# Performance work log

Measured on AMD Instinct MI355X. Metric: run time of the kernel, lower is better.

Reference implementation:

```python
import jax, jax.numpy as jnp
import numpy as np

D_MODEL = 1024
NUM_HEADS = 16
D_FF = 4096
NEG_INF = -1e9


def _linear_params(key, d_in, d_out):
    kw, kb = jax.random.split(key)
    bound = 1.0 / np.sqrt(d_in)
    W = jax.random.uniform(kw, (d_in, d_out), jnp.float32, -bound, bound)
    b = jax.random.uniform(kb, (d_out,), jnp.float32, -bound, bound)
    return W, b


def setup_inputs() -> dict:
    key = jax.random.key(0)
    ks = jax.random.split(key, 8)
    B, S = 2, 2048
    x = jax.random.normal(ks[0], (B, S, D_MODEL), jnp.float32)
    # causal mask: 1 = attend, 0 = masked
    mask = jnp.tril(jnp.ones((S, S), jnp.bool_))[None, :, :]
    Wq, bq = _linear_params(ks[1], D_MODEL, D_MODEL)
    Wk, bk = _linear_params(ks[2], D_MODEL, D_MODEL)
    Wv, bv = _linear_params(ks[3], D_MODEL, D_MODEL)
    Wo, bo = _linear_params(ks[4], D_MODEL, D_MODEL)
    W1, b1 = _linear_params(ks[5], D_MODEL, D_FF)
    W2, b2 = _linear_params(ks[6], D_FF, D_MODEL)
    ln1_g = jnp.ones((D_MODEL,), jnp.float32)
    ln1_b = jnp.zeros((D_MODEL,), jnp.float32)
    ln2_g = jnp.ones((D_MODEL,), jnp.float32)
    ln2_b = jnp.zeros((D_MODEL,), jnp.float32)
    return {"x": x, "mask": mask,
            "Wq": Wq, "bq": bq, "Wk": Wk, "bk": bk, "Wv": Wv, "bv": bv,
            "Wo": Wo, "bo": bo, "W1": W1, "b1": b1, "W2": W2, "b2": b2,
            "ln1_g": ln1_g, "ln1_b": ln1_b, "ln2_g": ln2_g, "ln2_b": ln2_b}


def layer_norm(x, g, b, eps=1e-5):
    mu = jnp.mean(x, axis=-1, keepdims=True)
    var = jnp.mean(jnp.square(x - mu), axis=-1, keepdims=True)
    return (x - mu) * jax.lax.rsqrt(var + eps) * g + b


def attention(xn, mask, Wq, bq, Wk, bk, Wv, bv, Wo, bo):
    B, S, D = xn.shape
    H, dk = NUM_HEADS, D // NUM_HEADS
    q = (xn @ Wq + bq).reshape(B, S, H, dk).transpose(0, 2, 1, 3)  # [B,H,S,dk]
    k = (xn @ Wk + bk).reshape(B, S, H, dk).transpose(0, 2, 1, 3)
    v = (xn @ Wv + bv).reshape(B, S, H, dk).transpose(0, 2, 1, 3)
    scores = jnp.einsum("bhsd,bhtd->bhst", q, k) / jnp.sqrt(jnp.float32(dk))
    scores = jnp.where(mask[:, None, :, :], scores, NEG_INF)
    attn = jax.nn.softmax(scores, axis=-1)
    out = jnp.einsum("bhst,bhtd->bhsd", attn, v)  # [B,H,S,dk]
    out = out.transpose(0, 2, 1, 3).reshape(B, S, D)
    return out @ Wo + bo


def reference(x, mask, Wq, bq, Wk, bk, Wv, bv, Wo, bo, W1, b1, W2, b2,
              ln1_g, ln1_b, ln2_g, ln2_b):
    # pre-norm MHA + residual (dropout = identity at eval)
    h = x + attention(layer_norm(x, ln1_g, ln1_b), mask,
                      Wq, bq, Wk, bk, Wv, bv, Wo, bo)
    # pre-norm FFN + residual
    ff = jax.nn.relu(layer_norm(h, ln2_g, ln2_b) @ W1 + b1) @ W2 + b2
    return h + ff
```

## Files before the change

### kernel.cpp

```cpp
#include <hip/hip_runtime.h>

typedef unsigned short u16;
typedef __attribute__((ext_vector_type(8))) short    s16x8;
typedef __attribute__((ext_vector_type(8))) unsigned short u16x8;
typedef __attribute__((ext_vector_type(4))) float    f32x4;

typedef __attribute__((address_space(1))) const void gvoid_c;
typedef __attribute__((address_space(3))) void       lvoid;

__device__ __forceinline__ float b2f(u16 x) {
    return __builtin_bit_cast(float, (unsigned)x << 16);
}
__device__ __forceinline__ u16 f2bf(float f) {
    unsigned u = __builtin_bit_cast(unsigned, f);
    return (u16)((u + 0x7FFFu + ((u >> 16) & 1u)) >> 16);
}
__device__ __forceinline__ u16 f2bf_trunc(float f) {
    return (u16)(__builtin_bit_cast(unsigned, f) >> 16);
}
__device__ __forceinline__ void gld16(const void* g, void* l) {
    __builtin_amdgcn_global_load_lds((gvoid_c*)g, (lvoid*)l, 16, 0, 0);
}

__global__ __launch_bounds__(256) void transpose_all(
    const float* __restrict__ Wq, const float* __restrict__ Wk,
    const float* __restrict__ Wv, const float* __restrict__ Wo,
    const float* __restrict__ W1, const float* __restrict__ W2,
    const float* __restrict__ bq, const float* __restrict__ bk,
    const float* __restrict__ bv,
    u16* __restrict__ Wqkv_t, u16* __restrict__ Wo_t,
    u16* __restrict__ W1_t, u16* __restrict__ W2_t, float* __restrict__ bqkv)
{
    __shared__ u16 tile[32][33];
    int id = blockIdx.x;
    if (id >= 12288) {
        int i = (id - 12288) * 256 + threadIdx.x;
        bqkv[i] = (i < 1024) ? bq[i] : (i < 2048 ? bk[i - 1024] : bv[i - 2048]);
        return;
    }
    const float* src; u16* dst; int R, C, bx, by;
    if (id < 4096) {
        int m = id >> 10, r = id & 1023;
        bx = r & 31; by = r >> 5; R = 1024; C = 1024;
        src = (m == 0) ? Wq : (m == 1) ? Wk : (m == 2) ? Wv : Wo;
        dst = (m == 0) ? Wqkv_t : (m == 1) ? Wqkv_t + 1024 * 1024
            : (m == 2) ? Wqkv_t + 2048 * 1024 : Wo_t;
    } else if (id < 8192) {
        int r = id - 4096; bx = r & 127; by = r >> 7; R = 1024; C = 4096;
        src = W1; dst = W1_t;
    } else {
        int r = id - 8192; bx = r & 31; by = r >> 5; R = 4096; C = 1024;
        src = W2; dst = W2_t;
    }
    int tx = threadIdx.x & 31, ty = threadIdx.x >> 5;
    int c0 = bx * 32, r0 = by * 32;
#pragma unroll
    for (int i = 0; i < 32; i += 8)
        tile[ty + i][tx] = f2bf(src[(size_t)(r0 + ty + i) * C + c0 + tx]);
    __syncthreads();
#pragma unroll
    for (int i = 0; i < 32; i += 8)
        dst[(size_t)(c0 + ty + i) * R + r0 + tx] = tile[tx][ty + i];
}

__global__ __launch_bounds__(256) void ln_k(
    const float* __restrict__ in, const float* __restrict__ gg,
    const float* __restrict__ bb, u16* __restrict__ out)
{
    const int D = 1024;
    int row  = blockIdx.x * 4 + (threadIdx.x >> 6);
    int lane = threadIdx.x & 63;
    const float* ip = in + (size_t)row * D;
    float v[16];
#pragma unroll
    for (int cc = 0; cc < 4; cc++) {
        f32x4 t = *(const f32x4*)(ip + cc * 256 + lane * 4);
#pragma unroll
        for (int i = 0; i < 4; i++) v[cc * 4 + i] = t[i];
    }
    float s1 = 0.f, s2 = 0.f;
#pragma unroll
    for (int i = 0; i < 16; i++) { s1 += v[i]; s2 += v[i] * v[i]; }
#pragma unroll
    for (int m = 1; m < 64; m <<= 1) { s1 += __shfl_xor(s1, m); s2 += __shfl_xor(s2, m); }
    float mu   = s1 * (1.f / 1024.f);
    float var  = s2 * (1.f / 1024.f) - mu * mu;
    float rstd = rsqrtf(var + 1e-5f);
#pragma unroll
    for (int cc = 0; cc < 4; cc++) {
        int e = cc * 256 + lane * 4;
        f32x4 gv = *(const f32x4*)(gg + e);
        f32x4 bv = *(const f32x4*)(bb + e);
        u16 o[4];
#pragma unroll
        for (int i = 0; i < 4; i++)
            o[i] = f2bf((v[cc * 4 + i] - mu) * rstd * gv[i] + bv[i]);
        *(__attribute__((ext_vector_type(4))) unsigned short*)(out + (size_t)row * D + e) =
            (__attribute__((ext_vector_type(4))) unsigned short){o[0], o[1], o[2], o[3]};
    }
}

template <int BN, int RES, bool RELU, bool OUTF32>
__global__ __launch_bounds__(256) void gemm2(
    const u16* __restrict__ A, const u16* __restrict__ Bt,
    const float* __restrict__ bias, const float* __restrict__ res,
    void* __restrict__ out, int M, int N, int K)
{
    constexpr int NFR = BN / 32;
    __shared__ u16 As[2][4096];
    __shared__ u16 Bs[2][BN * 32];
    int tid = threadIdx.x, wave = tid >> 6, lane = tid & 63;
    int g = lane >> 4, c = lane & 15;
    int wm = wave >> 1, wn = wave & 1;

    int gx = gridDim.x, nwg = gx * gridDim.y;
    int id = blockIdx.y * gx + blockIdx.x;
    int swz = (id & 7) * (nwg >> 3) + (id >> 3);
    int m0 = (swz / gx) * 128, n0 = (swz % gx) * BN;

    f32x4 acc[4][NFR];
#pragma unroll
    for (int m = 0; m < 4; m++)
#pragma unroll
        for (int n = 0; n < NFR; n++) acc[m][n] = (f32x4){0, 0, 0, 0};

    int ch0 = wave * 128 + lane, ch1 = ch0 + 64;
    const u16* Ag0 = A + (size_t)(m0 + (ch0 >> 2)) * K + (ch0 & 3) * 8;
    const u16* Ag1 = A + (size_t)(m0 + (ch1 >> 2)) * K + (ch1 & 3) * 8;
    const u16* Bg0;
    const u16* Bg1 = nullptr;
    if constexpr (BN == 128) {
        Bg0 = Bt + (size_t)(n0 + (ch0 >> 2)) * K + (ch0 & 3) * 8;
        Bg1 = Bt + (size_t)(n0 + (ch1 >> 2)) * K + (ch1 & 3) * 8;
    } else {
        int chb = wave * 64 + lane;
        Bg0 = Bt + (size_t)(n0 + (chb >> 2)) * K + (chb & 3) * 8;
    }

    auto stage = [&](int buf, int kk) {
        gld16(Ag0 + kk, &As[buf][wave * 1024]);
        gld16(Ag1 + kk, &As[buf][wave * 1024 + 512]);
        if constexpr (BN == 128) {
            gld16(Bg0 + kk, &Bs[buf][wave * 1024]);
            gld16(Bg1 + kk, &Bs[buf][wave * 1024 + 512]);
        } else {
            gld16(Bg0 + kk, &Bs[buf][wave * 512]);
        }
    };

    int nt = K / 32;
    stage(0, 0);
    __syncthreads();
    int cur = 0;
    for (int t = 0; t < nt; t++) {
        if (t + 1 < nt) stage(cur ^ 1, (t + 1) * 32);
        s16x8 af[4], bfr[NFR];
#pragma unroll
        for (int m = 0; m < 4; m++)
            af[m] = *(const s16x8*)&As[cur][(wm * 64 + m * 16 + c) * 32 + g * 8];
#pragma unroll
        for (int n = 0; n < NFR; n++)
            bfr[n] = *(const s16x8*)&Bs[cur][(wn * (BN / 2) + n * 16 + c) * 32 + g * 8];
        __builtin_amdgcn_s_setprio(1);
#pragma unroll
        for (int m = 0; m < 4; m++)
#pragma unroll
            for (int n = 0; n < NFR; n++)
                acc[m][n] = __builtin_amdgcn_mfma_f32_16x16x32_bf16(af[m], bfr[n], acc[m][n], 0, 0, 0);
        __builtin_amdgcn_s_setprio(0);
        __syncthreads();
        cur ^= 1;
    }

#pragma unroll
    for (int n = 0; n < NFR; n++) {
        int col = n0 + wn * (BN / 2) + n * 16 + c;
        float bb = bias[col];
#pragma unroll
        for (int m = 0; m < 4; m++) {
#pragma unroll
            for (int j = 0; j < 4; j++) {
                int row = m0 + wm * 64 + m * 16 + g * 4 + j;
                float v = acc[m][n][j] + bb;
                if constexpr (RES == 2) v += res[(size_t)row * N + col];
                if constexpr (RELU) v = fmaxf(v, 0.f);
                if constexpr (OUTF32) ((float*)out)[(size_t)row * N + col] = v;
                else                  ((u16*)out)[(size_t)row * N + col] = f2bf(v);
            }
        }
    }
}

__global__ __launch_bounds__(256) void gemm_n64_k64(
    const u16* __restrict__ A, const u16* __restrict__ Bt,
    const float* __restrict__ bias, const float* __restrict__ res,
    float* __restrict__ out, int M, int N, int K)
{
    __shared__ u16 As[2][8192];
    __shared__ u16 Bs[2][4096];
    int tid = threadIdx.x, wave = tid >> 6, lane = tid & 63;
    int g = lane >> 4, c = lane & 15;
    int wm = wave >> 1, wn = wave & 1;

    int gx = gridDim.x, nwg = gx * gridDim.y;
    int id = blockIdx.y * gx + blockIdx.x;
    int swz = (id & 7) * (nwg >> 3) + (id >> 3);
    int m0 = (swz / gx) * 128, n0 = (swz % gx) * 64;

    f32x4 acc[4][2];
#pragma unroll
    for (int m = 0; m < 4; m++)
#pragma unroll
        for (int n = 0; n < 2; n++) acc[m][n] = (f32x4){0, 0, 0, 0};

    const u16* asrc[4];
#pragma unroll
    for (int k = 0; k < 4; k++) {
        int ch = k * 256 + tid, row = ch >> 3, c8 = ch & 7;
        asrc[k] = A + (size_t)(m0 + row) * K + ((c8 ^ (row & 7)) * 8);
    }
    const u16* bsrc[2];
#pragma unroll
    for (int k = 0; k < 2; k++) {
        int ch = k * 256 + tid, row = ch >> 3, c8 = ch & 7;
        bsrc[k] = Bt + (size_t)(n0 + row) * K + ((c8 ^ (row & 7)) * 8);
    }

    auto stage = [&](int buf, int k0) {
#pragma unroll
        for (int k = 0; k < 4; k++)
            gld16(asrc[k] + k0, &As[buf][(k * 256 + wave * 64) * 8]);
#pragma unroll
        for (int k = 0; k < 2; k++)
            gld16(bsrc[k] + k0, &Bs[buf][(k * 256 + wave * 64) * 8]);
    };

    int nt = K / 64;
    stage(0, 0);
    __syncthreads();
    int cur = 0;
    int x7 = c & 7;
    for (int t = 0; t < nt; t++) {
        if (t + 1 < nt) stage(cur ^ 1, (t + 1) * 64);
        s16x8 af[2][4], bfr[2][2];
#pragma unroll
        for (int kk = 0; kk < 2; kk++) {
#pragma unroll
            for (int m = 0; m < 4; m++)
                af[kk][m] = *(const s16x8*)&As[cur][(wm * 64 + m * 16 + c) * 64 + ((kk * 4 + g) ^ x7) * 8];
#pragma unroll
            for (int n = 0; n < 2; n++)
                bfr[kk][n] = *(const s16x8*)&Bs[cur][(wn * 32 + n * 16 + c) * 64 + ((kk * 4 + g) ^ x7) * 8];
        }
        __builtin_amdgcn_s_setprio(1);
#pragma unroll
        for (int kk = 0; kk < 2; kk++)
#pragma unroll
            for (int m = 0; m < 4; m++)
#pragma unroll
                for (int n = 0; n < 2; n++)
                    acc[m][n] = __builtin_amdgcn_mfma_f32_16x16x32_bf16(af[kk][m], bfr[kk][n], acc[m][n], 0, 0, 0);
        __builtin_amdgcn_s_setprio(0);
        __syncthreads();
        cur ^= 1;
    }

#pragma unroll
    for (int n = 0; n < 2; n++) {
        int col = n0 + wn * 32 + n * 16 + c;
        float bb = bias[col];
#pragma unroll
        for (int m = 0; m < 4; m++) {
#pragma unroll
            for (int j = 0; j < 4; j++) {
                int row = m0 + wm * 64 + m * 16 + g * 4 + j;
                out[(size_t)row * N + col] = acc[m][n][j] + bb + res[(size_t)row * N + col];
            }
        }
    }
}

__global__ __launch_bounds__(256) void v_transpose(
    const u16* __restrict__ qkv, u16* __restrict__ vt)
{
    const int S = 2048, NC = 3072;
    __shared__ u16 tile[64][72];
    int st = blockIdx.x, bh = blockIdx.y, b = bh >> 4, h = bh & 15;
    int tid = threadIdx.x;
    int i = tid >> 3, cb8 = (tid & 7) * 8;
    const u16* src = qkv + (size_t)(b * S + st * 64) * NC + 2048 + h * 64;
    u16x8 a0 = *(const u16x8*)(src + (size_t)i * NC + cb8);
    u16x8 a1 = *(const u16x8*)(src + (size_t)(i + 32) * NC + cb8);
    *(u16x8*)&tile[i][cb8]      = a0;
    *(u16x8*)&tile[i + 32][cb8] = a1;
    __syncthreads();
    int d = tid >> 3, e8 = (tid & 7) * 8;
    int m = (d & 7) * 8;
#pragma unroll
    for (int rr = 0; rr < 2; rr++) {
        int r = d + rr * 32;
        u16x8 o;
#pragma unroll
        for (int j = 0; j < 8; j++) o[j] = tile[(e8 ^ m) + j][r];
        *(u16x8*)(vt + ((size_t)bh * 64 + r) * 2048 + st * 64 + e8) = o;
    }
}

__global__ __launch_bounds__(256) void attn_fwd4(
    const u16* __restrict__ qkv, const u16* __restrict__ vt,
    u16* __restrict__ o)
{
    const int S = 2048, NC = 3072;
    __shared__ u16 Ks[2][4096];
    __shared__ u16 Vs[2][4096];
    __shared__ u16 Plds[4][16][72];
    int qp = blockIdx.x, bh = blockIdx.y, b = bh >> 4, h = bh & 15;
    int tid = threadIdx.x, wave = tid >> 6, lane = tid & 63;
    int g = lane >> 4, c = lane & 15;
    int sr = tid >> 3, scb8 = (tid & 7) * 8;
    int mS = (sr & 7) * 8;
    int mR = (c & 7) * 8;

    const u16* kbase = qkv + (size_t)b * S * NC + 1024 + h * 64;
    const u16* vbase = vt + (size_t)bh * 64 * 2048;

    auto stageKV = [&](int buf, int t0) {
        gld16(kbase + (size_t)(t0 + sr)      * NC + (scb8 ^ mS), &Ks[buf][wave * 512]);
        gld16(kbase + (size_t)(t0 + sr + 32) * NC + (scb8 ^ mS), &Ks[buf][2048 + wave * 512]);
        gld16(vbase + (size_t)sr        * 2048 + t0 + scb8, &Vs[buf][wave * 512]);
        gld16(vbase + (size_t)(sr + 32) * 2048 + t0 + scb8, &Vs[buf][2048 + wave * 512]);
    };

#pragma unroll 1
    for (int ph = 0; ph < 2; ph++) {
        int qt = ph ? qp : 31 - qp;
        int q0 = qt * 64 + wave * 16;
        const u16* qptr = qkv + (size_t)(b * S + q0 + c) * NC + h * 64;
        s16x8 qf0 = *(const s16x8*)(qptr + g * 8);
        s16x8 qf1 = *(const s16x8*)(qptr + 32 + g * 8);

        float mr[4], lr[4];
        f32x4 acc[4];
#pragma unroll
        for (int j = 0; j < 4; j++) { mr[j] = -1e30f; lr[j] = 0.f; }
#pragma unroll
        for (int n = 0; n < 4; n++) acc[n] = (f32x4){0, 0, 0, 0};

        auto do_tile = [&](int cur, int t0, bool masked) __attribute__((always_inline)) {
            f32x4 s[4];
            __builtin_amdgcn_s_setprio(1);
#pragma unroll
            for (int kt = 0; kt < 4; kt++) {
                int r = kt * 16 + c;
                s16x8 kf0 = *(const s16x8*)&Ks[cur][r * 64 + ((g * 8) ^ mR)];
                s16x8 kf1 = *(const s16x8*)&Ks[cur][r * 64 + ((32 + g * 8) ^ mR)];
                f32x4 sv = (f32x4){0, 0, 0, 0};
                sv = __builtin_amdgcn_mfma_f32_16x16x32_bf16(qf0, kf0, sv, 0, 0, 0);
                sv = __builtin_amdgcn_mfma_f32_16x16x32_bf16(qf1, kf1, sv, 0, 0, 0);
                s[kt] = sv;
            }
            __builtin_amdgcn_s_setprio(0);
#pragma unroll
            for (int kt = 0; kt < 4; kt++) {
#pragma unroll
                for (int j = 0; j < 4; j++) {
                    if (masked) {
                        int kcol = t0 + kt * 16 + c;
                        int qrow = q0 + g * 4 + j;
                        s[kt][j] = (kcol <= qrow) ? s[kt][j] * 0.125f : -1e30f;
                    } else {
                        s[kt][j] *= 0.125f;
                    }
                }
            }
#pragma unroll
            for (int j = 0; j < 4; j++) {
                float tm = fmaxf(fmaxf(s[0][j], s[1][j]), fmaxf(s[2][j], s[3][j]));
#pragma unroll
                for (int m = 1; m < 16; m <<= 1) tm = fmaxf(tm, __shfl_xor(tm, m));
                float mnew = fmaxf(mr[j], tm);
                float corr = __expf(mr[j] - mnew);
                float rs = 0.f;
#pragma unroll
                for (int kt = 0; kt < 4; kt++) { float p = __expf(s[kt][j] - mnew); s[kt][j] = p; rs += p; }
#pragma unroll
                for (int m = 1; m < 16; m <<= 1) rs += __shfl_xor(rs, m);
                lr[j] = lr[j] * corr + rs;
                mr[j] = mnew;
#pragma unroll
                for (int n = 0; n < 4; n++) acc[n][j] *= corr;
            }
#pragma unroll
            for (int kt = 0; kt < 4; kt++)
#pragma unroll
                for (int j = 0; j < 4; j++)
                    Plds[wave][g * 4 + j][kt * 16 + c] = f2bf_trunc(s[kt][j]);
            s16x8 pa0 = *(const s16x8*)&Plds[wave][c][g * 8];
            s16x8 pa1 = *(const s16x8*)&Plds[wave][c][32 + g * 8];
            __builtin_amdgcn_s_setprio(1);
#pragma unroll
            for (int n = 0; n < 4; n++) {
                int r = n * 16 + c;
                s16x8 vb0 = *(const s16x8*)&Vs[cur][r * 64 + ((g * 8) ^ mR)];
                s16x8 vb1 = *(const s16x8*)&Vs[cur][r * 64 + ((32 + g * 8) ^ mR)];
                acc[n] = __builtin_amdgcn_mfma_f32_16x16x32_bf16(pa0, vb0, acc[n], 0, 0, 0);
                acc[n] = __builtin_amdgcn_mfma_f32_16x16x32_bf16(pa1, vb1, acc[n], 0, 0, 0);
            }
            __builtin_amdgcn_s_setprio(0);
        };

        __syncthreads();
        stageKV(0, 0);
        __syncthreads();
        int cur = 0;
        for (int t = 0; t < qt; t++) {
            stageKV(cur ^ 1, (t + 1) * 64);
            do_tile(cur, t * 64, false);
            __syncthreads();
            cur ^= 1;
        }
        do_tile(cur, qt * 64, true);

#pragma unroll
        for (int j = 0; j < 4; j++) {
            float inv = 1.f / lr[j];
            size_t rbase = (size_t)(b * S + q0 + g * 4 + j) * 1024 + h * 64;
#pragma unroll
            for (int n = 0; n < 4; n++)
                o[rbase + n * 16 + c] = f2bf(acc[n][j] * inv);
        }
    }
}

extern "C" void kernel_launch(void* const* d_in, const int* in_sizes, int n_in,
                              void* d_out, int out_size, void* d_ws, size_t ws_size,
                              hipStream_t stream)
{
    const float* x    = (const float*)d_in[0];
    const float* Wq   = (const float*)d_in[2];  const float* bq = (const float*)d_in[3];
    const float* Wk   = (const float*)d_in[4];  const float* bk = (const float*)d_in[5];
    const float* Wv   = (const float*)d_in[6];  const float* bv = (const float*)d_in[7];
    const float* Wo   = (const float*)d_in[8];  const float* bo = (const float*)d_in[9];
    const float* W1   = (const float*)d_in[10]; const float* b1 = (const float*)d_in[11];
    const float* W2   = (const float*)d_in[12]; const float* b2 = (const float*)d_in[13];
    const float* ln1g = (const float*)d_in[14]; const float* ln1b = (const float*)d_in[15];
    const float* ln2g = (const float*)d_in[16]; const float* ln2b = (const float*)d_in[17];

    unsigned char* ws = (unsigned char*)d_ws;
    u16*   Wqkv_t = (u16*)(ws + 0);
    u16*   Wo_t   = (u16*)(ws + 6291456);
    u16*   W1_t   = (u16*)(ws + 8388608);
    u16*   W2_t   = (u16*)(ws + 16777216);
    float* bqkv   = (float*)(ws + 25165824);
    u16*   lnbuf  = (u16*)(ws + 25178112);
    u16*   qkvbuf = (u16*)(ws + 33566720);
    u16*   attnb  = (u16*)(ws + 58732544);
    u16*   f1buf  = (u16*)(ws + 33566720);
    float* hbuf   = (float*)(ws + 67121152);
    u16*   vtbuf  = (u16*)(ws + 67121152);

    transpose_all<<<12300, 256, 0, stream>>>(Wq, Wk, Wv, Wo, W1, W2, bq, bk, bv,
                                             Wqkv_t, Wo_t, W1_t, W2_t, bqkv);

    ln_k<<<1024, 256, 0, stream>>>(x, ln1g, ln1b, lnbuf);
    gemm2<128, 0, false, false><<<dim3(24, 32), 256, 0, stream>>>(
        lnbuf, Wqkv_t, bqkv, nullptr, qkvbuf, 4096, 3072, 1024);
    v_transpose<<<dim3(32, 32), 256, 0, stream>>>(qkvbuf, vtbuf);
    attn_fwd4<<<dim3(16, 32), 256, 0, stream>>>(qkvbuf, vtbuf, attnb);

    gemm_n64_k64<<<dim3(16, 32), 256, 0, stream>>>(
        attnb, Wo_t, bo, x, hbuf, 4096, 1024, 1024);

    ln_k<<<1024, 256, 0, stream>>>(hbuf, ln2g, ln2b, lnbuf);
    gemm2<128, 0, true, false><<<dim3(32, 32), 256, 0, stream>>>(
        lnbuf, W1_t, b1, nullptr, f1buf, 4096, 4096, 1024);
    gemm_n64_k64<<<dim3(16, 32), 256, 0, stream>>>(
        f1buf, W2_t, b2, hbuf, (float*)d_out, 4096, 1024, 4096);
}
```

Measured before the change: 382.0 us.

## Split attention into one query tile per block with lazy softmax rescale

```diff
diff --git a/kernel.cpp b/kernel.cpp
--- a/kernel.cpp
+++ b/kernel.cpp
@@ -306,20 +306,23 @@
     }
 }
 
-__global__ __launch_bounds__(256) void attn_fwd4(
+__global__ __launch_bounds__(256) void attn_fwd5(
     const u16* __restrict__ qkv, const u16* __restrict__ vt,
     u16* __restrict__ o)
 {
     const int S = 2048, NC = 3072;
     __shared__ u16 Ks[2][4096];
     __shared__ u16 Vs[2][4096];
-    __shared__ u16 Plds[4][16][72];
-    int qp = blockIdx.x, bh = blockIdx.y, b = bh >> 4, h = bh & 15;
+    __shared__ u16 Plds[4][16][64];
+    int qt = 31 - blockIdx.x;
+    int bh = blockIdx.y, b = bh >> 4, h = bh & 15;
     int tid = threadIdx.x, wave = tid >> 6, lane = tid & 63;
     int g = lane >> 4, c = lane & 15;
     int sr = tid >> 3, scb8 = (tid & 7) * 8;
     int mS = (sr & 7) * 8;
     int mR = (c & 7) * 8;
+    int pW = ((g * 4) & 7) << 3;
+    int pR = (c & 7) << 3;
 
     const u16* kbase = qkv + (size_t)b * S * NC + 1024 + h * 64;
     const u16* vbase = vt + (size_t)bh * 64 * 2048;
@@ -331,104 +334,111 @@
         gld16(vbase + (size_t)(sr + 32) * 2048 + t0 + scb8, &Vs[buf][2048 + wave * 512]);
     };
 
-#pragma unroll 1
-    for (int ph = 0; ph < 2; ph++) {
-        int qt = ph ? qp : 31 - qp;
-        int q0 = qt * 64 + wave * 16;
-        const u16* qptr = qkv + (size_t)(b * S + q0 + c) * NC + h * 64;
-        s16x8 qf0 = *(const s16x8*)(qptr + g * 8);
-        s16x8 qf1 = *(const s16x8*)(qptr + 32 + g * 8);
-
-        float mr[4], lr[4];
-        f32x4 acc[4];
-#pragma unroll
-        for (int j = 0; j < 4; j++) { mr[j] = -1e30f; lr[j] = 0.f; }
-#pragma unroll
-        for (int n = 0; n < 4; n++) acc[n] = (f32x4){0, 0, 0, 0};
-
-        auto do_tile = [&](int cur, int t0, bool masked) __attribute__((always_inline)) {
-            f32x4 s[4];
-            __builtin_amdgcn_s_setprio(1);
-#pragma unroll
-            for (int kt = 0; kt < 4; kt++) {
-                int r = kt * 16 + c;
-                s16x8 kf0 = *(const s16x8*)&Ks[cur][r * 64 + ((g * 8) ^ mR)];
-                s16x8 kf1 = *(const s16x8*)&Ks[cur][r * 64 + ((32 + g * 8) ^ mR)];
-                f32x4 sv = (f32x4){0, 0, 0, 0};
-                sv = __builtin_amdgcn_mfma_f32_16x16x32_bf16(qf0, kf0, sv, 0, 0, 0);
-                sv = __builtin_amdgcn_mfma_f32_16x16x32_bf16(qf1, kf1, sv, 0, 0, 0);
-                s[kt] = sv;
-            }
-            __builtin_amdgcn_s_setprio(0);
-#pragma unroll
-            for (int kt = 0; kt < 4; kt++) {
-#pragma unroll
-                for (int j = 0; j < 4; j++) {
-                    if (masked) {
-                        int kcol = t0 + kt * 16 + c;
-                        int qrow = q0 + g * 4 + j;
-                        s[kt][j] = (kcol <= qrow) ? s[kt][j] * 0.125f : -1e30f;
-                    } else {
-                        s[kt][j] *= 0.125f;
-                    }
+    int q0 = qt * 64 + wave * 16;
+    const u16* qptr = qkv + (size_t)(b * S + q0 + c) * NC + h * 64;
+    s16x8 qf0 = *(const s16x8*)(qptr + g * 8);
+    s16x8 qf1 = *(const s16x8*)(qptr + 32 + g * 8);
+
+    float mr[4], lr[4];
+    f32x4 acc[4];
+#pragma unroll
+    for (int j = 0; j < 4; j++) { mr[j] = -1e30f; lr[j] = 0.f; }
+#pragma unroll
+    for (int n = 0; n < 4; n++) acc[n] = (f32x4){0, 0, 0, 0};
+
+    auto do_tile = [&](int cur, int t0, bool masked) __attribute__((always_inline)) {
+        f32x4 s[4];
+        __builtin_amdgcn_s_setprio(1);
+#pragma unroll
+        for (int kt = 0; kt < 4; kt++) {
+            int r = kt * 16 + c;
+            s16x8 kf0 = *(const s16x8*)&Ks[cur][r * 64 + ((g * 8) ^ mR)];
+            s16x8 kf1 = *(const s16x8*)&Ks[cur][r * 64 + ((32 + g * 8) ^ mR)];
+            f32x4 sv = (f32x4){0, 0, 0, 0};
+            sv = __builtin_amdgcn_mfma_f32_16x16x32_bf16(qf0, kf0, sv, 0, 0, 0);
+            sv = __builtin_amdgcn_mfma_f32_16x16x32_bf16(qf1, kf1, sv, 0, 0, 0);
+            s[kt] = sv;
+        }
+        __builtin_amdgcn_s_setprio(0);
+#pragma unroll
+        for (int kt = 0; kt < 4; kt++) {
+#pragma unroll
+            for (int j = 0; j < 4; j++) {
+                if (masked) {
+                    int kcol = t0 + kt * 16 + c;
+                    int qrow = q0 + g * 4 + j;
+                    s[kt][j] = (kcol <= qrow) ? s[kt][j] * 0.125f : -1e30f;
+                } else {
+                    s[kt][j] *= 0.125f;
                 }
             }
+        }
+        float tm4[4];
+#pragma unroll
+        for (int j = 0; j < 4; j++) {
+            float tm = fmaxf(fmaxf(s[0][j], s[1][j]), fmaxf(s[2][j], s[3][j]));
+#pragma unroll
+            for (int m = 1; m < 16; m <<= 1) tm = fmaxf(tm, __shfl_xor(tm, m));
+            tm4[j] = tm;
+        }
+        bool grow = (tm4[0] > mr[0]) | (tm4[1] > mr[1]) | (tm4[2] > mr[2]) | (tm4[3] > mr[3]);
+        if (__any(grow)) {
 #pragma unroll
             for (int j = 0; j < 4; j++) {
-                float tm = fmaxf(fmaxf(s[0][j], s[1][j]), fmaxf(s[2][j], s[3][j]));
-#pragma unroll
-                for (int m = 1; m < 16; m <<= 1) tm = fmaxf(tm, __shfl_xor(tm, m));
-                float mnew = fmaxf(mr[j], tm);
+                float mnew = fmaxf(mr[j], tm4[j]);
                 float corr = __expf(mr[j] - mnew);
-                float rs = 0.f;
-#pragma unroll
-                for (int kt = 0; kt < 4; kt++) { float p = __expf(s[kt][j] - mnew); s[kt][j] = p; rs += p; }
-#pragma unroll
-                for (int m = 1; m < 16; m <<= 1) rs += __shfl_xor(rs, m);
-                lr[j] = lr[j] * corr + rs;
                 mr[j] = mnew;
+                lr[j] *= corr;
 #pragma unroll
                 for (int n = 0; n < 4; n++) acc[n][j] *= corr;
             }
-#pragma unroll
-            for (int kt = 0; kt < 4; kt++)
-#pragma unroll
-                for (int j = 0; j < 4; j++)
-                    Plds[wave][g * 4 + j][kt * 16 + c] = f2bf_trunc(s[kt][j]);
-            s16x8 pa0 = *(const s16x8*)&Plds[wave][c][g * 8];
-            s16x8 pa1 = *(const s16x8*)&Plds[wave][c][32 + g * 8];
-            __builtin_amdgcn_s_setprio(1);
-#pragma unroll
-            for (int n = 0; n < 4; n++) {
-                int r = n * 16 + c;
-                s16x8 vb0 = *(const s16x8*)&Vs[cur][r * 64 + ((g * 8) ^ mR)];
-                s16x8 vb1 = *(const s16x8*)&Vs[cur][r * 64 + ((32 + g * 8) ^ mR)];
-                acc[n] = __builtin_amdgcn_mfma_f32_16x16x32_bf16(pa0, vb0, acc[n], 0, 0, 0);
-                acc[n] = __builtin_amdgcn_mfma_f32_16x16x32_bf16(pa1, vb1, acc[n], 0, 0, 0);
-            }
-            __builtin_amdgcn_s_setprio(0);
-        };
-
+        }
+#pragma unroll
+        for (int j = 0; j < 4; j++) {
+            float rs = 0.f;
+#pragma unroll
+            for (int kt = 0; kt < 4; kt++) { float p = __expf(s[kt][j] - mr[j]); s[kt][j] = p; rs += p; }
+#pragma unroll
+            for (int m = 1; m < 16; m <<= 1) rs += __shfl_xor(rs, m);
+            lr[j] += rs;
+        }
+#pragma unroll
+        for (int kt = 0; kt < 4; kt++)
+#pragma unroll
+            for (int j = 0; j < 4; j++)
+                Plds[wave][g * 4 + j][(kt * 16 + c) ^ (pW ^ ((j & 7) << 3) ? ((g * 4 + j) & 7) << 3 : ((g * 4 + j) & 7) << 3)] = f2bf_trunc(s[kt][j]);
+        s16x8 pa0 = *(const s16x8*)&Plds[wave][c][(g * 8) ^ pR];
+        s16x8 pa1 = *(const s16x8*)&Plds[wave][c][(32 + g * 8) ^ pR];
+        __builtin_amdgcn_s_setprio(1);
+#pragma unroll
+        for (int n = 0; n < 4; n++) {
+            int r = n * 16 + c;
+            s16x8 vb0 = *(const s16x8*)&Vs[cur][r * 64 + ((g * 8) ^ mR)];
+            s16x8 vb1 = *(const s16x8*)&Vs[cur][r * 64 + ((32 + g * 8) ^ mR)];
+            acc[n] = __builtin_amdgcn_mfma_f32_16x16x32_bf16(pa0, vb0, acc[n], 0, 0, 0);
+            acc[n] = __builtin_amdgcn_mfma_f32_16x16x32_bf16(pa1, vb1, acc[n], 0, 0, 0);
+        }
+        __builtin_amdgcn_s_setprio(0);
+    };
+
+    stageKV(0, 0);
+    __syncthreads();
+    int cur = 0;
+    for (int t = 0; t < qt; t++) {
+        stageKV(cur ^ 1, (t + 1) * 64);
+        do_tile(cur, t * 64, false);
         __syncthreads();
-        stageKV(0, 0);
-        __syncthreads();
-        int cur = 0;
-        for (int t = 0; t < qt; t++) {
-            stageKV(cur ^ 1, (t + 1) * 64);
-            do_tile(cur, t * 64, false);
-            __syncthreads();
-            cur ^= 1;
-        }
-        do_tile(cur, qt * 64, true);
-
-#pragma unroll
-        for (int j = 0; j < 4; j++) {
-            float inv = 1.f / lr[j];
-            size_t rbase = (size_t)(b * S + q0 + g * 4 + j) * 1024 + h * 64;
-#pragma unroll
-            for (int n = 0; n < 4; n++)
-                o[rbase + n * 16 + c] = f2bf(acc[n][j] * inv);
-        }
+        cur ^= 1;
+    }
+    do_tile(cur, qt * 64, true);
+
+#pragma unroll
+    for (int j = 0; j < 4; j++) {
+        float inv = 1.f / lr[j];
+        size_t rbase = (size_t)(b * S + q0 + g * 4 + j) * 1024 + h * 64;
+#pragma unroll
+        for (int n = 0; n < 4; n++)
+            o[rbase + n * 16 + c] = f2bf(acc[n][j] * inv);
     }
 }
 
@@ -466,7 +476,7 @@
     gemm2<128, 0, false, false><<<dim3(24, 32), 256, 0, stream>>>(
         lnbuf, Wqkv_t, bqkv, nullptr, qkvbuf, 4096, 3072, 1024);
     v_transpose<<<dim3(32, 32), 256, 0, stream>>>(qkvbuf, vtbuf);
-    attn_fwd4<<<dim3(16, 32), 256, 0, stream>>>(qkvbuf, vtbuf, attnb);
+    attn_fwd5<<<dim3(32, 32), 256, 0, stream>>>(qkvbuf, vtbuf, attnb);
 
     gemm_n64_k64<<<dim3(16, 32), 256, 0, stream>>>(
         attnb, Wo_t, bo, x, hbuf, 4096, 1024, 1024);
```

Measured after the change: 435.8 us. 14.1% more time.
